# Kernel tuning notes

Hardware: AMD Instinct MI355X
Metric: run time of the kernel (lower is better)

Reference implementation:

```python
import jax, jax.numpy as jnp
import numpy as np

NUM_HEADS = 32
HIDDEN = 4096
HEAD_DIM = HIDDEN // NUM_HEADS
BATCH = 1
SEQ = 2048


def setup_inputs() -> dict:
    key = jax.random.key(0)
    ks = jax.random.split(key, 8)
    hidden_states = jax.random.normal(ks[0], (BATCH, SEQ, HIDDEN), dtype=jnp.float32)
    residual = jax.random.normal(ks[1], (BATCH, SEQ, HIDDEN), dtype=jnp.float32)
    # BLOOM alibi: [batch*heads, 1, kv_len], broadcast over q_length in baddbmm
    alibi = jax.random.normal(ks[2], (BATCH * NUM_HEADS, 1, SEQ), dtype=jnp.float32) * 0.1
    # causal boolean mask: True = masked (filled with -inf before softmax)
    attention_mask = ~jnp.tril(jnp.ones((SEQ, SEQ), dtype=bool))[None, None, :, :]
    scale = 0.02
    Wqkv = jax.random.normal(ks[3], (3 * HIDDEN, HIDDEN), dtype=jnp.float32) * scale
    bqkv = jax.random.normal(ks[4], (3 * HIDDEN,), dtype=jnp.float32) * scale
    Wd = jax.random.normal(ks[5], (HIDDEN, HIDDEN), dtype=jnp.float32) * scale
    bd = jax.random.normal(ks[6], (HIDDEN,), dtype=jnp.float32) * scale
    return {"hidden_states": hidden_states, "residual": residual, "alibi": alibi,
            "attention_mask": attention_mask, "Wqkv": Wqkv, "bqkv": bqkv,
            "Wd": Wd, "bd": bd}


def reference(hidden_states, residual, alibi, attention_mask, Wqkv, bqkv, Wd, bd):
    B, S, H = hidden_states.shape
    nh, hd = NUM_HEADS, HEAD_DIM
    inv_norm = 1.0 / np.sqrt(hd).astype(np.float32)

    # fused QKV projection, BLOOM interleaved layout [B, S, nh, 3, hd]
    fused = hidden_states @ Wqkv.T + bqkv           # [B, S, 3H]
    fused = fused.reshape(B, S, nh, 3, hd)
    q = jnp.transpose(fused[..., 0, :], (0, 2, 1, 3))  # [B, nh, S, hd]
    k = jnp.transpose(fused[..., 1, :], (0, 2, 1, 3))  # [B, nh, S, hd]
    v = jnp.transpose(fused[..., 2, :], (0, 2, 1, 3))  # [B, nh, S, hd]

    # baddbmm: alibi + inv_norm * Q @ K^T
    alibi_b = alibi.reshape(B, nh, 1, S)                # broadcast over q_length
    scores = alibi_b + inv_norm * jnp.einsum('bhqd,bhkd->bhqk', q, k)
    scores = jnp.where(attention_mask, jnp.finfo(scores.dtype).min, scores)
    probs = jax.nn.softmax(scores, axis=-1)             # [B, nh, S, S]

    ctx = jnp.einsum('bhqk,bhkd->bhqd', probs, v)       # [B, nh, S, hd]
    ctx = jnp.transpose(ctx, (0, 2, 1, 3)).reshape(B, S, H)
    out = ctx @ Wd.T + bd
    return residual + out
```

## Files before the change

kernel.cpp:

```cpp
#include <hip/hip_runtime.h>


#define SEQL 2048
#define HIDN 4096
#define NHEAD 32
#define HDIM 128
#define H3 12288

typedef __bf16 bf16x8 __attribute__((ext_vector_type(8)));
typedef float f32x4 __attribute__((ext_vector_type(4)));
typedef unsigned short u16x8 __attribute__((ext_vector_type(8)));

__device__ __forceinline__ unsigned short f2bf(float f) {
  union { float f; unsigned u; } v; v.f = f;
  return (unsigned short)((v.u + 0x7FFFu + ((v.u >> 16) & 1u)) >> 16);
}

__device__ __forceinline__ void gload_lds16(const void* g, void* l) {
  __builtin_amdgcn_global_load_lds(
      (const __attribute__((address_space(1))) void*)g,
      (__attribute__((address_space(3))) void*)l, 16, 0, 0);
}

__global__ __launch_bounds__(256) void cvt_f32_bf16(
    const float* __restrict__ in, unsigned short* __restrict__ out, long long n) {
  long long i = ((long long)blockIdx.x * blockDim.x + threadIdx.x) * 8;
  long long stride = (long long)gridDim.x * blockDim.x * 8;
  for (; i < n; i += stride) {
    float4 a = *(const float4*)(in + i);
    float4 b = *(const float4*)(in + i + 4);
    u16x8 o;
    o[0] = f2bf(a.x); o[1] = f2bf(a.y); o[2] = f2bf(a.z); o[3] = f2bf(a.w);
    o[4] = f2bf(b.x); o[5] = f2bf(b.y); o[6] = f2bf(b.z); o[7] = f2bf(b.w);
    *(u16x8*)(out + i) = o;
  }
}

__global__ __launch_bounds__(512, 2) void gemm256_qkv(
    const unsigned short* __restrict__ A, const unsigned short* __restrict__ B,
    const float* __restrict__ bias,
    unsigned short* __restrict__ q_bf, unsigned short* __restrict__ k_bf,
    unsigned short* __restrict__ v_t) {
  __shared__ unsigned short lds[2][2][2][8192];

  const int tid = threadIdx.x;
  const int l = tid & 63;
  const int w = tid >> 6;
  const int K = HIDN;

  const int b = blockIdx.x;
  const int lin = (b & 7) * 48 + (b >> 3);
  const int tm0 = (lin & 7) * 256;
  const int tn0 = (lin >> 3) * 256;

  const int lr = l >> 3;
  const int lc = (l & 7) ^ lr;
  const int wm = (w >> 2) * 64;
  const int wn = (w & 3) * 32;

  f32x4 acc[2][2][4][2] = {};

  auto stageA = [&](int bf, int mh, int kt) {
#pragma unroll
    for (int i = 0; i < 2; ++i) {
      const int c = w * 2 + i;
      gload_lds16(&A[(long long)(tm0 + mh * 128 + c * 8 + lr) * K + kt + lc * 8],
                  (char*)&lds[bf][0][mh][0] + c * 1024);
    }
  };
  auto stageB = [&](int bf, int nh, int kt) {
#pragma unroll
    for (int i = 0; i < 2; ++i) {
      const int c = w * 2 + i;
      gload_lds16(&B[(long long)(tn0 + nh * 128 + c * 8 + lr) * K + kt + lc * 8],
                  (char*)&lds[bf][1][nh][0] + c * 1024);
    }
  };

  stageA(0, 0, 0);
  stageB(0, 0, 0);
  stageB(0, 1, 0);
  stageA(0, 1, 0);
  asm volatile("s_waitcnt vmcnt(4)" ::: "memory");
  __builtin_amdgcn_s_barrier();

  const int NT = K / 64;
  for (int t = 0; t < NT; ++t) {
    const int bf = t & 1, nb = bf ^ 1;
    const int kt1 = (t + 1) * 64;
    const bool pf = (t + 1 < NT);
#pragma unroll
    for (int ph = 0; ph < 4; ++ph) {
      const int mh = ph >> 1, nh = ph & 1;
      bf16x8 af[4][2], bfr[2][2];
#pragma unroll
      for (int mi = 0; mi < 4; ++mi) {
        const int r = wm + mi * 16 + (l & 15);
#pragma unroll
        for (int kk = 0; kk < 2; ++kk)
          af[mi][kk] = *(const bf16x8*)((const char*)&lds[bf][0][mh][0] +
              r * 128 + ((kk * 64 + (l >> 4) * 16) ^ ((l & 7) << 4)));
      }
#pragma unroll
      for (int ni = 0; ni < 2; ++ni) {
        const int r = wn + ni * 16 + (l & 15);
#pragma unroll
        for (int kk = 0; kk < 2; ++kk)
          bfr[ni][kk] = *(const bf16x8*)((const char*)&lds[bf][1][nh][0] +
              r * 128 + ((kk * 64 + (l >> 4) * 16) ^ ((l & 7) << 4)));
      }
      if (ph == 0) {
        if (pf) { stageA(nb, 0, kt1); asm volatile("s_waitcnt vmcnt(4)" ::: "memory"); }
        else    { asm volatile("s_waitcnt vmcnt(2)" ::: "memory"); }
      } else if (ph == 1) {
        if (pf) { stageB(nb, 0, kt1); asm volatile("s_waitcnt vmcnt(4)" ::: "memory"); }
        else    { asm volatile("s_waitcnt vmcnt(0)" ::: "memory"); }
      } else if (ph == 2) {
        if (pf) { stageB(nb, 1, kt1); }
      } else {
        if (pf) { stageA(nb, 1, kt1); asm volatile("s_waitcnt vmcnt(4)" ::: "memory"); }
      }
      __builtin_amdgcn_s_barrier();
      asm volatile("s_waitcnt lgkmcnt(0)" ::: "memory");
      __builtin_amdgcn_s_setprio(1);
#pragma unroll
      for (int kk = 0; kk < 2; ++kk)
#pragma unroll
        for (int mi = 0; mi < 4; ++mi)
#pragma unroll
          for (int ni = 0; ni < 2; ++ni)
            acc[mh][nh][mi][ni] = __builtin_amdgcn_mfma_f32_16x16x32_bf16(
                af[mi][kk], bfr[ni][kk], acc[mh][nh][mi][ni], 0, 0, 0);
      __builtin_amdgcn_s_setprio(0);
      __builtin_amdgcn_s_barrier();
    }
  }

#pragma unroll
  for (int mh = 0; mh < 2; ++mh)
#pragma unroll
    for (int nh = 0; nh < 2; ++nh)
#pragma unroll
      for (int mi = 0; mi < 4; ++mi)
#pragma unroll
        for (int ni = 0; ni < 2; ++ni) {
          const int col = tn0 + nh * 128 + wn + ni * 16 + (l & 15);
          const float bv = bias[col];
          const int head = col / 384;
          const int rem = col - head * 384;
          const int which = rem >> 7;
          const int d = rem & 127;
#pragma unroll
          for (int r = 0; r < 4; ++r) {
            const int row = tm0 + mh * 128 + wm + mi * 16 + (l >> 4) * 4 + r;
            const unsigned short bv16 = f2bf(acc[mh][nh][mi][ni][r] + bv);
            if (which == 0)
              q_bf[(long long)(head * SEQL + row) * HDIM + d] = bv16;
            else if (which == 1)
              k_bf[(long long)(head * SEQL + row) * HDIM + d] = bv16;
            else
              v_t[(long long)(head * HDIM + d) * SEQL + row] = bv16;
          }
        }
}

__global__ __launch_bounds__(256) void gemm_nt_res(
    const unsigned short* __restrict__ A, const unsigned short* __restrict__ B,
    int M, int N, int K,
    const float* __restrict__ bias, const float* __restrict__ residual,
    float* __restrict__ outf) {
  __shared__ unsigned short As[128 * 64];
  __shared__ unsigned short Bs[128 * 64];

  const int tid = threadIdx.x;
  const int l = tid & 63;
  const int w = tid >> 6;
  const int wr = (w >> 1) * 64;
  const int wc = (w & 1) * 64;
  const int tm0 = blockIdx.x * 128;
  const int tn0 = blockIdx.y * 128;

  const int lr = l >> 3;
  const int lc = (l & 7) ^ lr;

  f32x4 acc[4][4] = {};

  for (int kt = 0; kt < K; kt += 64) {
    __syncthreads();
#pragma unroll
    for (int i = 0; i < 4; ++i) {
      const int row = w * 32 + i * 8 + lr;
      gload_lds16(&A[(long long)(tm0 + row) * K + kt + lc * 8],
                  (char*)As + (w * 4 + i) * 1024);
      gload_lds16(&B[(long long)(tn0 + row) * K + kt + lc * 8],
                  (char*)Bs + (w * 4 + i) * 1024);
    }
    __syncthreads();
#pragma unroll
    for (int kk = 0; kk < 2; ++kk) {
      const int colb = kk * 64 + (l >> 4) * 16;
      bf16x8 af[4], bfr[4];
#pragma unroll
      for (int m = 0; m < 4; ++m) {
        int row = wr + m * 16 + (l & 15);
        af[m] = *(const bf16x8*)((char*)As + row * 128 + (colb ^ ((row & 7) << 4)));
      }
#pragma unroll
      for (int n = 0; n < 4; ++n) {
        int row = wc + n * 16 + (l & 15);
        bfr[n] = *(const bf16x8*)((char*)Bs + row * 128 + (colb ^ ((row & 7) << 4)));
      }
#pragma unroll
      for (int m = 0; m < 4; ++m)
#pragma unroll
        for (int n = 0; n < 4; ++n)
          acc[m][n] = __builtin_amdgcn_mfma_f32_16x16x32_bf16(af[m], bfr[n], acc[m][n], 0, 0, 0);
    }
  }

#pragma unroll
  for (int m = 0; m < 4; ++m)
#pragma unroll
    for (int n = 0; n < 4; ++n) {
      const int col = tn0 + wc + n * 16 + (l & 15);
      const float bv = bias[col];
#pragma unroll
      for (int r = 0; r < 4; ++r) {
        const int rowg = tm0 + wr + m * 16 + (l >> 4) * 4 + r;
        const long long idx = (long long)rowg * N + col;
        outf[idx] = acc[m][n][r] + bv + residual[idx];
      }
    }
}

__global__ __launch_bounds__(256) void attn_fwd(
    const unsigned short* __restrict__ q_bf, const unsigned short* __restrict__ k_bf,
    const unsigned short* __restrict__ v_t, const float* __restrict__ alibi,
    unsigned short* __restrict__ ctx_bf) {
  __shared__ unsigned short Ks[64 * 128];
  __shared__ unsigned short Vs[128 * 64];
  __shared__ unsigned short Ps[4][16 * 64];
  __shared__ float Al[SEQL];

  const int tid = threadIdx.x;
  const int l = tid & 63;
  const int w = tid >> 6;
  const int h = blockIdx.x;
  const int qt = blockIdx.y * 64;
  const int qw = qt + w * 16;

  for (int i = tid; i < SEQL; i += 256) Al[i] = alibi[h * SEQL + i];

  bf16x8 qf[4];
  {
    const unsigned short* qp =
        &q_bf[(long long)(h * SEQL + qw + (l & 15)) * HDIM + (l >> 4) * 8];
#pragma unroll
    for (int kk = 0; kk < 4; ++kk) qf[kk] = *(const bf16x8*)(qp + kk * 32);
  }

  f32x4 oacc[8] = {};
  float mrun[4] = {-__builtin_inff(), -__builtin_inff(), -__builtin_inff(), -__builtin_inff()};
  float lrun[4] = {0.f, 0.f, 0.f, 0.f};
  const float inv_norm = 0.08838834764831845f;

  const int kR = l >> 4, kC = l & 15;
  const int vR = l >> 3, vC = (l & 7) ^ vR;

  const int ntiles = blockIdx.y + 1;
  for (int t = 0; t < ntiles; ++t) {
    const int kv0 = t * 64;
    __syncthreads();
#pragma unroll
    for (int i = 0; i < 4; ++i) {
      const int krow = w * 16 + i * 4 + kR;
      const int ksrc = kC ^ ((i & 1) * 4 + kR);
      gload_lds16(&k_bf[(long long)(h * SEQL + kv0 + krow) * HDIM + ksrc * 8],
                  (char*)Ks + (w * 4 + i) * 1024);
      const int vrow = w * 32 + i * 8 + vR;
      gload_lds16(&v_t[(long long)(h * HDIM + vrow) * SEQL + kv0 + vC * 8],
                  (char*)Vs + (w * 4 + i) * 1024);
    }
    __syncthreads();

    f32x4 sacc[4] = {};
#pragma unroll
    for (int kk = 0; kk < 4; ++kk) {
      const int colb = kk * 64 + (l >> 4) * 16;
#pragma unroll
      for (int n = 0; n < 4; ++n) {
        int row = n * 16 + (l & 15);
        bf16x8 kf = *(const bf16x8*)((char*)Ks + row * 256 + (colb ^ ((row & 7) << 4)));
        sacc[n] = __builtin_amdgcn_mfma_f32_16x16x32_bf16(qf[kk], kf, sacc[n], 0, 0, 0);
      }
    }

    float sc[4][4];
#pragma unroll
    for (int n = 0; n < 4; ++n) {
      const int kv = kv0 + n * 16 + (l & 15);
      const float al = Al[kv];
#pragma unroll
      for (int r = 0; r < 4; ++r) {
        const int qrow = qw + (l >> 4) * 4 + r;
        float v = al + inv_norm * sacc[n][r];
        sc[n][r] = (kv > qrow) ? -__builtin_inff() : v;
      }
    }

#pragma unroll
    for (int r = 0; r < 4; ++r) {
      float m0 = fmaxf(fmaxf(sc[0][r], sc[1][r]), fmaxf(sc[2][r], sc[3][r]));
      m0 = fmaxf(m0, __shfl_xor(m0, 1, 64));
      m0 = fmaxf(m0, __shfl_xor(m0, 2, 64));
      m0 = fmaxf(m0, __shfl_xor(m0, 4, 64));
      m0 = fmaxf(m0, __shfl_xor(m0, 8, 64));
      const float mnew = fmaxf(mrun[r], m0);
      float p0 = 0.f;
#pragma unroll
      for (int n = 0; n < 4; ++n) {
        const float pv = __expf(sc[n][r] - mnew);
        sc[n][r] = pv;
        p0 += pv;
      }
      p0 += __shfl_xor(p0, 1, 64);
      p0 += __shfl_xor(p0, 2, 64);
      p0 += __shfl_xor(p0, 4, 64);
      p0 += __shfl_xor(p0, 8, 64);
      const float scale = __expf(mrun[r] - mnew);
      mrun[r] = mnew;
      lrun[r] = lrun[r] * scale + p0;
#pragma unroll
      for (int n2 = 0; n2 < 8; ++n2) oacc[n2][r] *= scale;
    }

#pragma unroll
    for (int n = 0; n < 4; ++n)
#pragma unroll
      for (int r = 0; r < 4; ++r) {
        const int row = (l >> 4) * 4 + r;
        const int colp = n * 16 + (l & 15);
        *(unsigned short*)((char*)Ps[w] + row * 128 + ((colp * 2) ^ ((row & 7) << 4))) =
            f2bf(sc[n][r]);
      }
    __threadfence_block();
    bf16x8 pf[2];
#pragma unroll
    for (int kk2 = 0; kk2 < 2; ++kk2) {
      const int row = l & 15;
      const int colb = kk2 * 64 + (l >> 4) * 16;
      pf[kk2] = *(const bf16x8*)((char*)Ps[w] + row * 128 + (colb ^ ((row & 7) << 4)));
    }

#pragma unroll
    for (int n2 = 0; n2 < 8; ++n2) {
#pragma unroll
      for (int kk2 = 0; kk2 < 2; ++kk2) {
        const int row = n2 * 16 + (l & 15);
        const int colb = kk2 * 64 + (l >> 4) * 16;
        bf16x8 vf = *(const bf16x8*)((char*)Vs + row * 128 + (colb ^ ((row & 7) << 4)));
        oacc[n2] = __builtin_amdgcn_mfma_f32_16x16x32_bf16(pf[kk2], vf, oacc[n2], 0, 0, 0);
      }
    }
  }

#pragma unroll
  for (int n2 = 0; n2 < 8; ++n2)
#pragma unroll
    for (int r = 0; r < 4; ++r) {
      const int qrow = qw + (l >> 4) * 4 + r;
      const int col = h * HDIM + n2 * 16 + (l & 15);
      ctx_bf[(long long)qrow * HIDN + col] = f2bf(oacc[n2][r] / lrun[r]);
    }
}

extern "C" void kernel_launch(void* const* d_in, const int* in_sizes, int n_in,
                              void* d_out, int out_size, void* d_ws, size_t ws_size,
                              hipStream_t stream) {
  const float* hidden = (const float*)d_in[0];
  const float* residual = (const float*)d_in[1];
  const float* alibi = (const float*)d_in[2];
  const float* Wqkv = (const float*)d_in[4];
  const float* bqkv = (const float*)d_in[5];
  const float* Wd = (const float*)d_in[6];
  const float* bd = (const float*)d_in[7];
  float* out = (float*)d_out;

  char* ws = (char*)d_ws;
  const size_t MB16 = 16777216;
  unsigned short* q_bf = (unsigned short*)(ws);
  unsigned short* k_bf = (unsigned short*)(ws + MB16);
  unsigned short* v_t = (unsigned short*)(ws + 2 * MB16);
  unsigned short* hid_bf = (unsigned short*)(ws + 3 * MB16);
  unsigned short* wqkv_bf = (unsigned short*)(ws + 4 * MB16);
  unsigned short* wd_bf = (unsigned short*)(ws + 4 * MB16);
  unsigned short* ctx_bf = (unsigned short*)(ws + 4 * MB16 + 33554432);

  cvt_f32_bf16<<<4096, 256, 0, stream>>>(hidden, hid_bf, (long long)SEQL * HIDN);
  cvt_f32_bf16<<<24576, 256, 0, stream>>>(Wqkv, wqkv_bf, (long long)H3 * HIDN);

  gemm256_qkv<<<384, 512, 0, stream>>>(hid_bf, wqkv_bf, bqkv, q_bf, k_bf, v_t);

  cvt_f32_bf16<<<8192, 256, 0, stream>>>(Wd, wd_bf, (long long)HIDN * HIDN);

  attn_fwd<<<dim3(NHEAD, SEQL / 64), 256, 0, stream>>>(q_bf, k_bf, v_t, alibi, ctx_bf);

  gemm_nt_res<<<dim3(SEQL / 128, HIDN / 128), 256, 0, stream>>>(
      ctx_bf, wd_bf, SEQL, HIDN, HIDN, bd, residual, out);
}
```

Measured before the change: 541.0 us.

## Software-pipeline LDS fragment reads with MFMA in QKV GEMM via register double-buffering

Restructures the QKV GEMM main loop so each wave loads its A/B fragments from LDS into separate register sets while MFMAs on the previous fragments run. The next tile's first fragments are prefetched at the end of each iteration. It also remaps wave-to-subtile ownership so each wave reuses A and B fragments across quadrants instead of reloading them every phase. The cost is more live registers at 2 blocks per CU, which risks spills, plus tricky waitcnt and barrier ordering that could expose races.

```diff
diff --git a/kernel.cpp b/kernel.cpp
--- a/kernel.cpp
+++ b/kernel.cpp
@@ -21,6 +21,10 @@
       (const __attribute__((address_space(1))) void*)g,
       (__attribute__((address_space(3))) void*)l, 16, 0, 0);
 }
+
+#define BAR() __builtin_amdgcn_s_barrier()
+#define SCHED0() __builtin_amdgcn_sched_barrier(0x7)
+#define VM(n) asm volatile("s_waitcnt vmcnt(" #n ")" ::: "memory")
 
 __global__ __launch_bounds__(256) void cvt_f32_bf16(
     const float* __restrict__ in, unsigned short* __restrict__ out, long long n) {
@@ -41,7 +45,8 @@
     const float* __restrict__ bias,
     unsigned short* __restrict__ q_bf, unsigned short* __restrict__ k_bf,
     unsigned short* __restrict__ v_t) {
-  __shared__ unsigned short lds[2][2][2][8192];
+  __shared__ unsigned short Ab[2][2][8192];
+  __shared__ unsigned short Bb[2][2][8192];
 
   const int tid = threadIdx.x;
   const int l = tid & 63;
@@ -55,85 +60,94 @@
 
   const int lr = l >> 3;
   const int lc = (l & 7) ^ lr;
-  const int wm = (w >> 2) * 64;
-  const int wn = (w & 3) * 32;
+  const int wm = w >> 2;
+  const int wn = w & 3;
+  const int bhalf = wn >> 1;
+  const int brow0 = (wn & 1) * 64;
 
   f32x4 acc[2][2][4][2] = {};
-
-  auto stageA = [&](int bf, int mh, int kt) {
+  bf16x8 A0s[4][2], A1s[4][2], B0s[2][2], B1s[2][2];
+
+  auto stA = [&](int tt, int h) {
 #pragma unroll
     for (int i = 0; i < 2; ++i) {
       const int c = w * 2 + i;
-      gload_lds16(&A[(long long)(tm0 + mh * 128 + c * 8 + lr) * K + kt + lc * 8],
-                  (char*)&lds[bf][0][mh][0] + c * 1024);
+      gload_lds16(&A[(long long)(tm0 + h * 128 + c * 8 + lr) * K + tt * 64 + lc * 8],
+                  (char*)&Ab[tt & 1][h][0] + c * 1024);
     }
   };
-  auto stageB = [&](int bf, int nh, int kt) {
+  auto stB = [&](int tt, int h) {
 #pragma unroll
     for (int i = 0; i < 2; ++i) {
       const int c = w * 2 + i;
-      gload_lds16(&B[(long long)(tn0 + nh * 128 + c * 8 + lr) * K + kt + lc * 8],
-                  (char*)&lds[bf][1][nh][0] + c * 1024);
+      gload_lds16(&B[(long long)(tn0 + h * 128 + c * 8 + lr) * K + tt * 64 + lc * 8],
+                  (char*)&Bb[tt & 1][h][0] + c * 1024);
     }
   };
-
-  stageA(0, 0, 0);
-  stageB(0, 0, 0);
-  stageB(0, 1, 0);
-  stageA(0, 1, 0);
-  asm volatile("s_waitcnt vmcnt(4)" ::: "memory");
-  __builtin_amdgcn_s_barrier();
+  auto rdA = [&](bf16x8 (&dst)[4][2], int bufi, int mh) {
+#pragma unroll
+    for (int mi = 0; mi < 4; ++mi) {
+      const int r = mh * 64 + mi * 16 + (l & 15);
+#pragma unroll
+      for (int kk = 0; kk < 2; ++kk)
+        dst[mi][kk] = *(const bf16x8*)((const char*)&Ab[bufi][wm][0] +
+            r * 128 + ((kk * 64 + (l >> 4) * 16) ^ ((r & 7) << 4)));
+    }
+  };
+  auto rdB = [&](bf16x8 (&dst)[2][2], int bufi, int nh) {
+#pragma unroll
+    for (int ni = 0; ni < 2; ++ni) {
+      const int r = brow0 + nh * 32 + ni * 16 + (l & 15);
+#pragma unroll
+      for (int kk = 0; kk < 2; ++kk)
+        dst[ni][kk] = *(const bf16x8*)((const char*)&Bb[bufi][bhalf][0] +
+            r * 128 + ((kk * 64 + (l >> 4) * 16) ^ ((r & 7) << 4)));
+    }
+  };
+
+#define MFMA16(As_, Bs_, mh_, nh_)                                            \
+  __builtin_amdgcn_s_setprio(1);                                              \
+  _Pragma("unroll") for (int kk = 0; kk < 2; ++kk)                            \
+    _Pragma("unroll") for (int mi = 0; mi < 4; ++mi)                          \
+      _Pragma("unroll") for (int ni = 0; ni < 2; ++ni)                        \
+        acc[mh_][nh_][mi][ni] = __builtin_amdgcn_mfma_f32_16x16x32_bf16(      \
+            As_[mi][kk], Bs_[ni][kk], acc[mh_][nh_][mi][ni], 0, 0, 0);        \
+  __builtin_amdgcn_s_setprio(0);
+
+  stA(0, 0); stB(0, 0); stB(0, 1); stA(0, 1);
+  VM(2);
+  BAR();
+  SCHED0();
+  rdA(A0s, 0, 0);
+  rdB(B0s, 0, 0);
+  SCHED0();
 
   const int NT = K / 64;
   for (int t = 0; t < NT; ++t) {
-    const int bf = t & 1, nb = bf ^ 1;
-    const int kt1 = (t + 1) * 64;
-    const bool pf = (t + 1 < NT);
-#pragma unroll
-    for (int ph = 0; ph < 4; ++ph) {
-      const int mh = ph >> 1, nh = ph & 1;
-      bf16x8 af[4][2], bfr[2][2];
-#pragma unroll
-      for (int mi = 0; mi < 4; ++mi) {
-        const int r = wm + mi * 16 + (l & 15);
-#pragma unroll
-        for (int kk = 0; kk < 2; ++kk)
-          af[mi][kk] = *(const bf16x8*)((const char*)&lds[bf][0][mh][0] +
-              r * 128 + ((kk * 64 + (l >> 4) * 16) ^ ((l & 7) << 4)));
-      }
-#pragma unroll
-      for (int ni = 0; ni < 2; ++ni) {
-        const int r = wn + ni * 16 + (l & 15);
-#pragma unroll
-        for (int kk = 0; kk < 2; ++kk)
-          bfr[ni][kk] = *(const bf16x8*)((const char*)&lds[bf][1][nh][0] +
-              r * 128 + ((kk * 64 + (l >> 4) * 16) ^ ((l & 7) << 4)));
-      }
-      if (ph == 0) {
-        if (pf) { stageA(nb, 0, kt1); asm volatile("s_waitcnt vmcnt(4)" ::: "memory"); }
-        else    { asm volatile("s_waitcnt vmcnt(2)" ::: "memory"); }
-      } else if (ph == 1) {
-        if (pf) { stageB(nb, 0, kt1); asm volatile("s_waitcnt vmcnt(4)" ::: "memory"); }
-        else    { asm volatile("s_waitcnt vmcnt(0)" ::: "memory"); }
-      } else if (ph == 2) {
-        if (pf) { stageB(nb, 1, kt1); }
-      } else {
-        if (pf) { stageA(nb, 1, kt1); asm volatile("s_waitcnt vmcnt(4)" ::: "memory"); }
-      }
-      __builtin_amdgcn_s_barrier();
-      asm volatile("s_waitcnt lgkmcnt(0)" ::: "memory");
-      __builtin_amdgcn_s_setprio(1);
-#pragma unroll
-      for (int kk = 0; kk < 2; ++kk)
-#pragma unroll
-        for (int mi = 0; mi < 4; ++mi)
-#pragma unroll
-          for (int ni = 0; ni < 2; ++ni)
-            acc[mh][nh][mi][ni] = __builtin_amdgcn_mfma_f32_16x16x32_bf16(
-                af[mi][kk], bfr[ni][kk], acc[mh][nh][mi][ni], 0, 0, 0);
-      __builtin_amdgcn_s_setprio(0);
-      __builtin_amdgcn_s_barrier();
-    }
+    const int bf = t & 1;
+    const bool pf = (t + 1) < NT;
+    if (pf) { stA(t + 1, 0); VM(4); } else { VM(2); }
+    BAR(); SCHED0();
+    MFMA16(A0s, B0s, 0, 0);
+    rdB(B1s, bf, 1);
+    SCHED0(); BAR();
+    if (pf) { stB(t + 1, 0); VM(4); } else { VM(0); }
+    BAR(); SCHED0();
+    MFMA16(A0s, B1s, 0, 1);
+    rdA(A1s, bf, 1);
+    SCHED0(); BAR();
+    if (pf) { stB(t + 1, 1); }
+    BAR(); SCHED0();
+    MFMA16(A1s, B0s, 1, 0);
+    SCHED0(); BAR();
+    if (pf) { stA(t + 1, 1); VM(4); }
+    BAR(); SCHED0();
+    MFMA16(A1s, B1s, 1, 1);
+    if (pf) {
+      rdA(A0s, bf ^ 1, 0);
+      rdB(B0s, bf ^ 1, 0);
+    }
+    SCHED0(); BAR();
   }
 
 #pragma unroll
@@ -144,7 +158,7 @@
       for (int mi = 0; mi < 4; ++mi)
 #pragma unroll
         for (int ni = 0; ni < 2; ++ni) {
-          const int col = tn0 + nh * 128 + wn + ni * 16 + (l & 15);
+          const int col = tn0 + wn * 64 + nh * 32 + ni * 16 + (l & 15);
           const float bv = bias[col];
           const int head = col / 384;
           const int rem = col - head * 384;
@@ -152,7 +166,7 @@
           const int d = rem & 127;
 #pragma unroll
           for (int r = 0; r < 4; ++r) {
-            const int row = tm0 + mh * 128 + wm + mi * 16 + (l >> 4) * 4 + r;
+            const int row = tm0 + wm * 128 + mh * 64 + mi * 16 + (l >> 4) * 4 + r;
             const unsigned short bv16 = f2bf(acc[mh][nh][mi][ni][r] + bv);
             if (which == 0)
               q_bf[(long long)(head * SEQL + row) * HDIM + d] = bv16;
```

New measurement: 514.0 us. -5.0%, faster.
